# Kernel tuning notes

Measured on AMD Instinct MI355X. Metric: run time of the kernel, lower is better.

Reference implementation:

```python
import jax, jax.numpy as jnp
import numpy as np

NBITS = 8          # attn_nbits
GROUP = 32         # per-group size along head_dim for Q/K quantizers
H = 16             # num_heads
EPS = 1e-8


def _ste(x, q):
    # straight-through estimator: forward=q, backward=identity
    return x + jax.lax.stop_gradient(q - x)


def pg_dynamic_quant(x, group_size=GROUP, nbits=NBITS):
    """Per-group symmetric dynamic fake-quant along last dim (ActPGDynamicQuantizer)."""
    qmax = 2.0 ** (nbits - 1) - 1
    lead, D = x.shape[:-1], x.shape[-1]
    xg = x.reshape(*lead, D // group_size, group_size)
    s = jnp.maximum(jnp.max(jnp.abs(xg), axis=-1, keepdims=True) / qmax, EPS)
    q = jnp.clip(jnp.round(xg / s), -qmax - 1.0, qmax) * s
    return _ste(x, q.reshape(x.shape))


def dynamic_quant(x, axis=2, nbits=NBITS):
    """Symmetric dynamic fake-quant, scale shared along `axis` (ActDynamicQuantizer)."""
    qmax = 2.0 ** (nbits - 1) - 1
    s = jnp.maximum(jnp.max(jnp.abs(x), axis=axis, keepdims=True) / qmax, EPS)
    q = jnp.clip(jnp.round(x / s), -qmax - 1.0, qmax) * s
    return _ste(x, q)


def static_scale_quant(x, nbits=NBITS):
    """Unsigned static-scale fake-quant for softmax map in [0,1] (ActStaticScaleQuantizer)."""
    qmax = 2.0 ** nbits - 1
    q = jnp.clip(jnp.round(x * qmax), 0.0, qmax) / qmax
    return _ste(x, q)


def setup_inputs() -> dict:
    key = jax.random.key(0)
    ks = jax.random.split(key, 7)
    B, L, C = 4, 1024, 1024
    return {
        "x":         jax.random.normal(ks[0], (B, L, C), jnp.float32),
        "attn_bias": jax.random.normal(ks[1], (1, 1, L, L), jnp.float32) * 0.1,
        "w_qkv":     jax.random.normal(ks[2], (3 * C, C), jnp.float32) * 0.02,
        "q_bias":    jax.random.normal(ks[3], (C,), jnp.float32) * 0.02,
        "v_bias":    jax.random.normal(ks[4], (C,), jnp.float32) * 0.02,
        "w_proj":    jax.random.normal(ks[5], (C, C), jnp.float32) * 0.02,
        "b_proj":    jax.random.normal(ks[6], (C,), jnp.float32) * 0.02,
    }


def reference(x, attn_bias, w_qkv, q_bias, v_bias, w_proj, b_proj):
    B, L, C = x.shape
    D = C // H
    scale = D ** -0.5
    # qkv projection: bias-free linear + concat(q_bias, zeros_k, v_bias)
    bias = jnp.concatenate([q_bias, jnp.zeros_like(q_bias), v_bias])
    qkv = (x @ w_qkv.T + bias).reshape(B, L, 3, H, D)
    q, k, v = jnp.transpose(qkv, (2, 0, 3, 1, 4))  # each [B,H,L,D]
    # inline fake-quantization (MODE 0 inference path)
    qq = pg_dynamic_quant(q)
    kk = pg_dynamic_quant(k)
    vv = dynamic_quant(v, axis=2)
    attn = jnp.einsum('bhld,bhmd->bhlm', qq * scale, kk) + attn_bias  # [B,H,L,L]
    a = jax.nn.softmax(attn, axis=-1)
    a = static_scale_quant(a)
    out = jnp.einsum('bhlm,bhmd->bhld', a, vv)
    out = jnp.transpose(out, (0, 2, 1, 3)).reshape(B, L, C)
    return out @ w_proj.T + b_proj
```

## Files before the change

kernel.cpp:

```cpp
#include <hip/hip_runtime.h>


typedef unsigned short u16;
typedef unsigned int u32;
typedef __attribute__((ext_vector_type(8))) _Float16 half8;
typedef __attribute__((ext_vector_type(4))) float f32x4;

__device__ __forceinline__ u16 f2b(float f) {
    u32 i;
    __builtin_memcpy(&i, &f, 4);
    return (u16)((i + 0x7FFFu + ((i >> 16) & 1u)) >> 16);
}

__device__ __forceinline__ void split16(float v, u16& hi, u16& lo) {
    _Float16 h = (_Float16)v;
    _Float16 l = (_Float16)(v - (float)h);
    __builtin_memcpy(&hi, &h, 2);
    __builtin_memcpy(&lo, &l, 2);
}

__device__ __forceinline__ int dot4(int a, int b, int c) {
#if __has_builtin(__builtin_amdgcn_sdot4)
    return __builtin_amdgcn_sdot4(a, b, c, false);
#else
    int r = c;
    r += ((a << 24) >> 24) * ((b << 24) >> 24);
    r += ((a << 16) >> 24) * ((b << 16) >> 24);
    r += ((a << 8) >> 24) * ((b << 8) >> 24);
    r += (a >> 24) * (b >> 24);
    return r;
#endif
}

__global__ __launch_bounds__(256) void cvt_bf16w(u16* __restrict__ dst,
                                                 const float* __restrict__ src, int n) {
    int i = (blockIdx.x * 256 + threadIdx.x) * 4;
    if (i + 3 < n) {
        float4 v = *(const float4*)(src + i);
        ushort4 o;
        o.x = f2b(v.x); o.y = f2b(v.y); o.z = f2b(v.z); o.w = f2b(v.w);
        *(ushort4*)(dst + i) = o;
    }
}

__global__ __launch_bounds__(256) void gemm_qkv3(const float* __restrict__ A,
                                                 const float* __restrict__ Bm,
                                                 const float* __restrict__ qbias,
                                                 const float* __restrict__ vbias,
                                                 float* __restrict__ qws,
                                                 float* __restrict__ kws,
                                                 float* __restrict__ vws) {
    __shared__ u16 Ah[128 * 32], Al[128 * 32], Bh[128 * 32], Bl[128 * 32];
    const int t = threadIdx.x;
    const int lane = t & 63, w = t >> 6;
    const int wm = w >> 1, wn = w & 1;
    const int srow = t >> 2, scol = (t & 3) * 8;
    const int lm = lane & 15, lk = (lane >> 4) * 8;
    const int bm = blockIdx.y, bn = blockIdx.x;

    const float* ap = A + (size_t)(bm * 128 + srow) * 1024 + scol;
    const float* bp = Bm + (size_t)(bn * 128 + srow) * 1024 + scol;

    double dacc[4][4][4];
#pragma unroll
    for (int i = 0; i < 4; i++)
#pragma unroll
        for (int j = 0; j < 4; j++)
#pragma unroll
            for (int r = 0; r < 4; r++) dacc[i][j][r] = 0.0;

    for (int slab = 0; slab < 8; slab++) {
        f32x4 acc[4][4];
#pragma unroll
        for (int i = 0; i < 4; i++)
#pragma unroll
            for (int j = 0; j < 4; j++) acc[i][j] = (f32x4){0.f, 0.f, 0.f, 0.f};

        for (int kc = 0; kc < 4; kc++) {
            const int k0 = slab * 128 + kc * 32;
            float vreg[4][8];
#pragma unroll
            for (int e = 0; e < 4; e++) {
                const float* src = (e < 2) ? (ap + (e & 1) * (size_t)64 * 1024 + k0)
                                           : (bp + (e & 1) * (size_t)64 * 1024 + k0);
                float4 v0 = *(const float4*)(src);
                float4 v1 = *(const float4*)(src + 4);
                vreg[e][0] = v0.x; vreg[e][1] = v0.y; vreg[e][2] = v0.z; vreg[e][3] = v0.w;
                vreg[e][4] = v1.x; vreg[e][5] = v1.y; vreg[e][6] = v1.z; vreg[e][7] = v1.w;
            }
            __syncthreads();
#pragma unroll
            for (int e = 0; e < 4; e++) {
                union { u16 us[8]; uint4 v; } ph, pl;
#pragma unroll
                for (int j = 0; j < 8; j++) split16(vreg[e][j], ph.us[j], pl.us[j]);
                u16* dh = (e < 2) ? Ah : Bh;
                u16* dl = (e < 2) ? Al : Bl;
                int row = srow + (e & 1) * 64;
                *(uint4*)(dh + row * 32 + scol) = ph.v;
                *(uint4*)(dl + row * 32 + scol) = pl.v;
            }
            __syncthreads();

            half8 fah[4], fal[4], fbh[4], fbl[4];
#pragma unroll
            for (int i = 0; i < 4; i++) {
                int ra = (wm * 64 + i * 16 + lm) * 32 + lk;
                int rb = (wn * 64 + i * 16 + lm) * 32 + lk;
                fah[i] = *(const half8*)(Ah + ra);
                fal[i] = *(const half8*)(Al + ra);
                fbh[i] = *(const half8*)(Bh + rb);
                fbl[i] = *(const half8*)(Bl + rb);
            }
#pragma unroll
            for (int mi = 0; mi < 4; mi++)
#pragma unroll
                for (int ni = 0; ni < 4; ni++) {
                    acc[mi][ni] = __builtin_amdgcn_mfma_f32_16x16x32_f16(
                        fal[mi], fbh[ni], acc[mi][ni], 0, 0, 0);
                    acc[mi][ni] = __builtin_amdgcn_mfma_f32_16x16x32_f16(
                        fah[mi], fbl[ni], acc[mi][ni], 0, 0, 0);
                    acc[mi][ni] = __builtin_amdgcn_mfma_f32_16x16x32_f16(
                        fah[mi], fbh[ni], acc[mi][ni], 0, 0, 0);
                }
        }
#pragma unroll
        for (int i = 0; i < 4; i++)
#pragma unroll
            for (int j = 0; j < 4; j++)
#pragma unroll
                for (int r = 0; r < 4; r++) dacc[i][j][r] += (double)acc[i][j][r];
    }

    const int rbase = bm * 128 + wm * 64 + (lane >> 4) * 4;
    const int cbase = bn * 128 + wn * 64 + lm;
#pragma unroll
    for (int mi = 0; mi < 4; mi++)
#pragma unroll
        for (int ni = 0; ni < 4; ni++) {
            int col = cbase + ni * 16;
            int sel = col >> 10, cc = col & 1023;
            double bias = (sel == 0) ? (double)qbias[cc]
                        : ((sel == 2) ? (double)vbias[cc] : 0.0);
            float* dst = (sel == 0) ? qws : ((sel == 1) ? kws : vws);
#pragma unroll
            for (int r = 0; r < 4; r++) {
                int row = rbase + mi * 16 + r;
                dst[(size_t)row * 1024 + cc] = (float)(dacc[mi][ni][r] + bias);
            }
        }
}

__global__ __launch_bounds__(256) void quant_qk(const float* __restrict__ pre,
                                                signed char* __restrict__ qout,
                                                double* __restrict__ sout) {
    size_t g = (size_t)blockIdx.x * 256 + threadIdx.x;
    const float* p = pre + g * 32;
    float v[32];
    float amax = 0.f;
#pragma unroll
    for (int i = 0; i < 8; i++) {
        float4 q4 = ((const float4*)p)[i];
        v[i * 4 + 0] = q4.x; v[i * 4 + 1] = q4.y; v[i * 4 + 2] = q4.z; v[i * 4 + 3] = q4.w;
        amax = fmaxf(amax, fmaxf(fmaxf(fabsf(q4.x), fabsf(q4.y)),
                                 fmaxf(fabsf(q4.z), fabsf(q4.w))));
    }
    double s = fmax((double)amax / 127.0, 1e-8);
    sout[g] = s;
    int pk[8];
#pragma unroll
    for (int i = 0; i < 8; i++) {
        int b0 = (int)fmin(fmax(rint((double)v[i * 4 + 0] / s), -128.0), 127.0);
        int b1 = (int)fmin(fmax(rint((double)v[i * 4 + 1] / s), -128.0), 127.0);
        int b2 = (int)fmin(fmax(rint((double)v[i * 4 + 2] / s), -128.0), 127.0);
        int b3 = (int)fmin(fmax(rint((double)v[i * 4 + 3] / s), -128.0), 127.0);
        pk[i] = (b0 & 255) | ((b1 & 255) << 8) | ((b2 & 255) << 16) | ((b3 & 255) << 24);
    }
    int4* d = (int4*)(qout + g * 32);
    d[0] = make_int4(pk[0], pk[1], pk[2], pk[3]);
    d[1] = make_int4(pk[4], pk[5], pk[6], pk[7]);
}

__global__ __launch_bounds__(256) void quant_k(const float* __restrict__ pre,
                                               int* __restrict__ kT,
                                               double* __restrict__ ksT) {
    size_t g = (size_t)blockIdx.x * 256 + threadIdx.x;
    const float* p = pre + g * 32;
    float v[32];
    float amax = 0.f;
#pragma unroll
    for (int i = 0; i < 8; i++) {
        float4 q4 = ((const float4*)p)[i];
        v[i * 4 + 0] = q4.x; v[i * 4 + 1] = q4.y; v[i * 4 + 2] = q4.z; v[i * 4 + 3] = q4.w;
        amax = fmaxf(amax, fmaxf(fmaxf(fabsf(q4.x), fabsf(q4.y)),
                                 fmaxf(fabsf(q4.z), fabsf(q4.w))));
    }
    double s = fmax((double)amax / 127.0, 1e-8);
    int pk[8];
#pragma unroll
    for (int i = 0; i < 8; i++) {
        int b0 = (int)fmin(fmax(rint((double)v[i * 4 + 0] / s), -128.0), 127.0);
        int b1 = (int)fmin(fmax(rint((double)v[i * 4 + 1] / s), -128.0), 127.0);
        int b2 = (int)fmin(fmax(rint((double)v[i * 4 + 2] / s), -128.0), 127.0);
        int b3 = (int)fmin(fmax(rint((double)v[i * 4 + 3] / s), -128.0), 127.0);
        pk[i] = (b0 & 255) | ((b1 & 255) << 8) | ((b2 & 255) << 16) | ((b3 & 255) << 24);
    }
    const int m = (int)((g >> 5) & 1023);
    const int b = (int)(g >> 15);
    const int sub = (int)(g & 31);
    const int h = sub >> 1, pp = sub & 1;
    const int bh = b * 16 + h;
    int* dst = kT + ((size_t)bh * 16 + pp * 8) * 1024 + m;
#pragma unroll
    for (int i = 0; i < 8; i++) dst[i * 1024] = pk[i];
    ksT[((size_t)bh * 2 + pp) * 1024 + m] = s;
}

__global__ __launch_bounds__(256) void vmax_part(const float* __restrict__ vws,
                                                 float* __restrict__ pmax) {
    const int lc = blockIdx.x, b = blockIdx.y, t = threadIdx.x;
#pragma unroll
    for (int j = 0; j < 4; j++) {
        int cc = t + j * 256;
        float mx = 0.f;
        for (int l = 0; l < 64; l++)
            mx = fmaxf(mx, fabsf(vws[((size_t)(b * 1024 + lc * 64 + l)) * 1024 + cc]));
        pmax[(size_t)(b * 16 + lc) * 1024 + cc] = mx;
    }
}

__global__ __launch_bounds__(256) void vmax_final(const float* __restrict__ pmax,
                                                  double* __restrict__ vs) {
    int id = blockIdx.x * 256 + threadIdx.x;
    int b = id >> 10, cc = id & 1023;
    float mx = 0.f;
#pragma unroll
    for (int p = 0; p < 16; p++)
        mx = fmaxf(mx, pmax[(size_t)(b * 16 + p) * 1024 + cc]);
    vs[id] = fmax((double)mx / 127.0, 1e-8);
}

__global__ __launch_bounds__(256) void vquant(float* __restrict__ vws,
                                              const double* __restrict__ vs) {
    size_t e = ((size_t)blockIdx.x * 256 + threadIdx.x) * 4;
    int b = (int)(e >> 20), cc = (int)(e & 1023);
    float4 v = *(const float4*)(vws + e);
    double s0 = vs[b * 1024 + cc], s1 = vs[b * 1024 + cc + 1];
    double s2 = vs[b * 1024 + cc + 2], s3 = vs[b * 1024 + cc + 3];
    float4 o;
    o.x = (float)(fmin(fmax(rint((double)v.x / s0), -128.0), 127.0) * s0);
    o.y = (float)(fmin(fmax(rint((double)v.y / s1), -128.0), 127.0) * s1);
    o.z = (float)(fmin(fmax(rint((double)v.z / s2), -128.0), 127.0) * s2);
    o.w = (float)(fmin(fmax(rint((double)v.w / s3), -128.0), 127.0) * s3);
    *(float4*)(vws + e) = o;
}

__global__ __launch_bounds__(256) void attn(const signed char* __restrict__ qint,
                                            const int* __restrict__ kT,
                                            const double* __restrict__ qs,
                                            const double* __restrict__ ksT,
                                            const float* __restrict__ vfq,
                                            const float* __restrict__ abias,
                                            u16* __restrict__ ctx) {
    __shared__ int    kTs[16][256];
    __shared__ double ks0s[256], ks1s[256];
    __shared__ unsigned short sidx[4][512];
    __shared__ float  sval[4][512];
    const int t = threadIdx.x;
    const int wv = t >> 6, lane = t & 63;
    const int qt = blockIdx.x, h = blockIdx.y, b = blockIdx.z;
    const int row = qt * 4 + wv;
    const size_t qrow = (size_t)(b * 1024 + row);
    const int bh = b * 16 + h;

    const int* qv = (const int*)(qint + qrow * 1024 + h * 64);
    int qd[16];
#pragma unroll
    for (int j = 0; j < 4; j++) {
        int4 tmp = ((const int4*)qv)[j];
        qd[j * 4 + 0] = tmp.x; qd[j * 4 + 1] = tmp.y;
        qd[j * 4 + 2] = tmp.z; qd[j * 4 + 3] = tmp.w;
    }
    const double sq0 = qs[qrow * 32 + 2 * h], sq1 = qs[qrow * 32 + 2 * h + 1];
    const int* kTg = kT + (size_t)bh * 16384;
    const double* ks0g = ksT + (size_t)(bh * 2) * 1024;
    const double* ks1g = ksT + (size_t)(bh * 2 + 1) * 1024;
    const float* ab = abias + (size_t)row * 1024;

    double sd[16];
    for (int c = 0; c < 4; c++) {
        if (c) __syncthreads();
        {
            const int j = t >> 4, seg = t & 15;
            const int4* src = (const int4*)(kTg + j * 1024 + c * 256 + seg * 16);
            int4 a0 = src[0], a1 = src[1], a2 = src[2], a3 = src[3];
            int4* dst = (int4*)(&kTs[j][seg * 16]);
            dst[0] = a0; dst[1] = a1; dst[2] = a2; dst[3] = a3;
            ks0s[t] = ks0g[c * 256 + t];
            ks1s[t] = ks1g[c * 256 + t];
        }
        __syncthreads();
#pragma unroll
        for (int s = 0; s < 4; s++) {
            const int ml = s * 64 + lane;
            int I0 = 0, I1 = 0;
#pragma unroll
            for (int j = 0; j < 8; j++)  I0 = dot4(qd[j], kTs[j][ml], I0);
#pragma unroll
            for (int j = 8; j < 16; j++) I1 = dot4(qd[j], kTs[j][ml], I1);
            sd[c * 4 + s] = 0.125 * (sq0 * ks0s[ml] * (double)I0
                                   + sq1 * ks1s[ml] * (double)I1)
                          + (double)ab[c * 256 + ml];
        }
    }

    double mx = sd[0];
#pragma unroll
    for (int it = 1; it < 16; it++) mx = fmax(mx, sd[it]);
#pragma unroll
    for (int off = 1; off < 64; off <<= 1) mx = fmax(mx, __shfl_xor(mx, off));
    double sum = 0.0;
#pragma unroll
    for (int it = 0; it < 16; it++) {
        double e = exp(sd[it] - mx);
        sd[it] = e;
        sum += e;
    }
#pragma unroll
    for (int off = 1; off < 64; off <<= 1) sum += __shfl_xor(sum, off);

    int base = 0;
#pragma unroll
    for (int it = 0; it < 16; it++) {
        double a = sd[it] / sum;
        double n = fmin(fmax(rint(a * 255.0), 0.0), 255.0);
        float af = (float)(n / 255.0);
        unsigned long long mk = __ballot(af != 0.f);
        if (af != 0.f) {
            int pos = base + (int)__popcll(mk & ((1ull << lane) - 1ull));
            sidx[wv][pos] = (unsigned short)(it * 64 + lane);
            sval[wv][pos] = af;
        }
        base += (int)__popcll(mk);
    }
    __syncthreads();

    float acc = 0.f;
    const float* vcol = vfq + ((size_t)b * 1024) * 1024 + h * 64 + lane;
    for (int j = 0; j < base; ++j) {
        int m = sidx[wv][j];
        float a = sval[wv][j];
        acc = fmaf(a, vcol[(size_t)m * 1024], acc);
    }
    ctx[qrow * 1024 + h * 64 + lane] = f2b(acc);
}

__global__ __launch_bounds__(256) void gemm_proj(const u16* __restrict__ ctx,
                                                 const u16* __restrict__ wproj,
                                                 const float* __restrict__ bproj,
                                                 float* __restrict__ out) {
    typedef __attribute__((ext_vector_type(8))) short short8;
    __shared__ u16 As[128 * 32], Bs[128 * 32];
    f32x4 acc[4][4];
#pragma unroll
    for (int i = 0; i < 4; i++)
#pragma unroll
        for (int j = 0; j < 4; j++) acc[i][j] = (f32x4){0.f, 0.f, 0.f, 0.f};

    const int t = threadIdx.x;
    const int lane = t & 63, w = t >> 6;
    const int wm = w >> 1, wn = w & 1;
    const int srow = t >> 2, scol = (t & 3) * 8;
    const int lm = lane & 15, lk = (lane >> 4) * 8;
    const int bm = blockIdx.y, bn = blockIdx.x;
    const u16* ap = ctx + (size_t)(bm * 128 + srow) * 1024 + scol;
    const u16* bp = wproj + (size_t)(bn * 128 + srow) * 1024 + scol;

    for (int k0 = 0; k0 < 1024; k0 += 32) {
        uint4 a0 = *(const uint4*)(ap + k0);
        uint4 a1 = *(const uint4*)(ap + (size_t)64 * 1024 + k0);
        uint4 b0 = *(const uint4*)(bp + k0);
        uint4 b1 = *(const uint4*)(bp + (size_t)64 * 1024 + k0);
        __syncthreads();
        *(uint4*)(As + srow * 32 + scol) = a0;
        *(uint4*)(As + (srow + 64) * 32 + scol) = a1;
        *(uint4*)(Bs + srow * 32 + scol) = b0;
        *(uint4*)(Bs + (srow + 64) * 32 + scol) = b1;
        __syncthreads();
        short8 af[4], bfr[4];
#pragma unroll
        for (int i = 0; i < 4; i++) {
            af[i]  = *(const short8*)(As + (wm * 64 + i * 16 + lm) * 32 + lk);
            bfr[i] = *(const short8*)(Bs + (wn * 64 + i * 16 + lm) * 32 + lk);
        }
#pragma unroll
        for (int mi = 0; mi < 4; mi++)
#pragma unroll
            for (int ni = 0; ni < 4; ni++)
                acc[mi][ni] = __builtin_amdgcn_mfma_f32_16x16x32_bf16(
                    af[mi], bfr[ni], acc[mi][ni], 0, 0, 0);
    }

    const int rbase = bm * 128 + wm * 64 + (lane >> 4) * 4;
    const int cbase = bn * 128 + wn * 64 + lm;
#pragma unroll
    for (int mi = 0; mi < 4; mi++)
#pragma unroll
        for (int ni = 0; ni < 4; ni++) {
            int col = cbase + ni * 16;
            float bias = bproj[col];
#pragma unroll
            for (int r = 0; r < 4; r++) {
                int row = rbase + mi * 16 + r;
                out[(size_t)row * 1024 + col] = acc[mi][ni][r] + bias;
            }
        }
}

extern "C" void kernel_launch(void* const* d_in, const int* in_sizes, int n_in,
                              void* d_out, int out_size, void* d_ws, size_t ws_size,
                              hipStream_t stream) {
    const float* x     = (const float*)d_in[0];
    const float* abias = (const float*)d_in[1];
    const float* wqkv  = (const float*)d_in[2];
    const float* qbias = (const float*)d_in[3];
    const float* vbias = (const float*)d_in[4];
    const float* wproj = (const float*)d_in[5];
    const float* bproj = (const float*)d_in[6];
    float* out = (float*)d_out;

    char* ws = (char*)d_ws;
    float*       qpre    = (float*)(ws + 0);
    float*       kpre    = (float*)(ws + 16777216);
    float*       vfq     = (float*)(ws + 33554432);
    u16*         wprojbf = (u16*)  (ws + 50331648);
    signed char* qint    = (signed char*)(ws + 52428800);
    int*         kT      = (int*)  (ws + 56623104);
    double*      qs      = (double*)(ws + 60817408);
    double*      ksT     = (double*)(ws + 61865984);
    double*      vs      = (double*)(ws + 62914560);
    float*       pmax    = (float*)(ws + 62947328);
    u16*         ctx     = (u16*)(ws + 0);

    cvt_bf16w<<<1024, 256, 0, stream>>>(wprojbf, wproj, 1048576);
    gemm_qkv3<<<dim3(24, 32), 256, 0, stream>>>(x, wqkv, qbias, vbias,
                                                qpre, kpre, vfq);
    quant_qk<<<512, 256, 0, stream>>>(qpre, qint, qs);
    quant_k<<<512, 256, 0, stream>>>(kpre, kT, ksT);
    vmax_part<<<dim3(16, 4), 256, 0, stream>>>(vfq, pmax);
    vmax_final<<<16, 256, 0, stream>>>(pmax, vs);
    vquant<<<4096, 256, 0, stream>>>(vfq, vs);
    attn<<<dim3(256, 16, 4), 256, 0, stream>>>(qint, kT, qs, ksT, vfq, abias, ctx);
    gemm_proj<<<dim3(8, 32), 256, 0, stream>>>(ctx, wprojbf, bproj, out);
}
```

Measured before the change: 586.5 us.

## Interleave quantized K as int4 per key and drop LDS staging in attention

Quantized K is rewritten into an interleaved layout so each key's 16 packed int8 words sit in four int4 groups. The attention kernel then reads K and the K scales straight from global memory per lane, removing the LDS tile staging and the block-wide barriers in the score loop. The sparse softmax index and value lists are packed into one u32 per entry, cutting LDS use, which may raise occupancy. The cost is that every wave now loads K from global or cache on its own instead of sharing one tile across the block.

Result: slower. 650.6 us (+10.9%).

```diff
diff --git a/kernel.cpp b/kernel.cpp
--- a/kernel.cpp
+++ b/kernel.cpp
@@ -210,9 +210,9 @@
     const int sub = (int)(g & 31);
     const int h = sub >> 1, pp = sub & 1;
     const int bh = b * 16 + h;
-    int* dst = kT + ((size_t)bh * 16 + pp * 8) * 1024 + m;
-#pragma unroll
-    for (int i = 0; i < 8; i++) dst[i * 1024] = pk[i];
+    int* dst = kT + (((size_t)bh * 4 + pp * 2) * 1024 + m) * 4;
+#pragma unroll
+    for (int i = 0; i < 8; i++) dst[(i >> 2) * 4096 + (i & 3)] = pk[i];
     ksT[((size_t)bh * 2 + pp) * 1024 + m] = s;
 }
 
@@ -256,16 +256,13 @@
 }
 
 __global__ __launch_bounds__(256) void attn(const signed char* __restrict__ qint,
-                                            const int* __restrict__ kT,
+                                            const int* __restrict__ kT4,
                                             const double* __restrict__ qs,
                                             const double* __restrict__ ksT,
                                             const float* __restrict__ vfq,
                                             const float* __restrict__ abias,
                                             u16* __restrict__ ctx) {
-    __shared__ int    kTs[16][256];
-    __shared__ double ks0s[256], ks1s[256];
-    __shared__ unsigned short sidx[4][512];
-    __shared__ float  sval[4][512];
+    __shared__ u32 packed[4][512];
     const int t = threadIdx.x;
     const int wv = t >> 6, lane = t & 63;
     const int qt = blockIdx.x, h = blockIdx.y, b = blockIdx.z;
@@ -282,36 +279,31 @@
         qd[j * 4 + 2] = tmp.z; qd[j * 4 + 3] = tmp.w;
     }
     const double sq0 = qs[qrow * 32 + 2 * h], sq1 = qs[qrow * 32 + 2 * h + 1];
-    const int* kTg = kT + (size_t)bh * 16384;
+    const int4* kB = (const int4*)kT4 + (size_t)bh * 4096;
     const double* ks0g = ksT + (size_t)(bh * 2) * 1024;
     const double* ks1g = ksT + (size_t)(bh * 2 + 1) * 1024;
     const float* ab = abias + (size_t)row * 1024;
 
     double sd[16];
-    for (int c = 0; c < 4; c++) {
-        if (c) __syncthreads();
-        {
-            const int j = t >> 4, seg = t & 15;
-            const int4* src = (const int4*)(kTg + j * 1024 + c * 256 + seg * 16);
-            int4 a0 = src[0], a1 = src[1], a2 = src[2], a3 = src[3];
-            int4* dst = (int4*)(&kTs[j][seg * 16]);
-            dst[0] = a0; dst[1] = a1; dst[2] = a2; dst[3] = a3;
-            ks0s[t] = ks0g[c * 256 + t];
-            ks1s[t] = ks1g[c * 256 + t];
-        }
-        __syncthreads();
-#pragma unroll
-        for (int s = 0; s < 4; s++) {
-            const int ml = s * 64 + lane;
-            int I0 = 0, I1 = 0;
-#pragma unroll
-            for (int j = 0; j < 8; j++)  I0 = dot4(qd[j], kTs[j][ml], I0);
-#pragma unroll
-            for (int j = 8; j < 16; j++) I1 = dot4(qd[j], kTs[j][ml], I1);
-            sd[c * 4 + s] = 0.125 * (sq0 * ks0s[ml] * (double)I0
-                                   + sq1 * ks1s[ml] * (double)I1)
-                          + (double)ab[c * 256 + ml];
-        }
+#pragma unroll
+    for (int it = 0; it < 16; it++) {
+        const int m = it * 64 + lane;
+        int4 k0 = kB[m];
+        int4 k1 = kB[1024 + m];
+        int4 k2 = kB[2048 + m];
+        int4 k3 = kB[3072 + m];
+        int I0 = 0, I1 = 0;
+        I0 = dot4(qd[0], k0.x, I0);  I0 = dot4(qd[1], k0.y, I0);
+        I0 = dot4(qd[2], k0.z, I0);  I0 = dot4(qd[3], k0.w, I0);
+        I0 = dot4(qd[4], k1.x, I0);  I0 = dot4(qd[5], k1.y, I0);
+        I0 = dot4(qd[6], k1.z, I0);  I0 = dot4(qd[7], k1.w, I0);
+        I1 = dot4(qd[8], k2.x, I1);  I1 = dot4(qd[9], k2.y, I1);
+        I1 = dot4(qd[10], k2.z, I1); I1 = dot4(qd[11], k2.w, I1);
+        I1 = dot4(qd[12], k3.x, I1); I1 = dot4(qd[13], k3.y, I1);
+        I1 = dot4(qd[14], k3.z, I1); I1 = dot4(qd[15], k3.w, I1);
+        sd[it] = 0.125 * (sq0 * ks0g[m] * (double)I0
+                        + sq1 * ks1g[m] * (double)I1)
+               + (double)ab[m];
     }
 
     double mx = sd[0];
@@ -333,13 +325,12 @@
 #pragma unroll
     for (int it = 0; it < 16; it++) {
         double a = sd[it] / sum;
-        double n = fmin(fmax(rint(a * 255.0), 0.0), 255.0);
-        float af = (float)(n / 255.0);
-        unsigned long long mk = __ballot(af != 0.f);
-        if (af != 0.f) {
+        double nd = fmin(fmax(rint(a * 255.0), 0.0), 255.0);
+        int ni = (int)nd;
+        unsigned long long mk = __ballot(ni != 0);
+        if (ni != 0) {
             int pos = base + (int)__popcll(mk & ((1ull << lane) - 1ull));
-            sidx[wv][pos] = (unsigned short)(it * 64 + lane);
-            sval[wv][pos] = af;
+            packed[wv][pos] = ((u32)ni << 16) | (u32)(it * 64 + lane);
         }
         base += (int)__popcll(mk);
     }
@@ -348,9 +339,9 @@
     float acc = 0.f;
     const float* vcol = vfq + ((size_t)b * 1024) * 1024 + h * 64 + lane;
     for (int j = 0; j < base; ++j) {
-        int m = sidx[wv][j];
-        float a = sval[wv][j];
-        acc = fmaf(a, vcol[(size_t)m * 1024], acc);
+        u32 p = packed[wv][j];
+        float a = (float)(p >> 16) / 255.0f;
+        acc = fmaf(a, vcol[(size_t)(p & 1023u) * 1024], acc);
     }
     ctx[qrow * 1024 + h * 64 + lane] = f2b(acc);
 }
@@ -435,7 +426,7 @@
     float*       vfq     = (float*)(ws + 33554432);
     u16*         wprojbf = (u16*)  (ws + 50331648);
     signed char* qint    = (signed char*)(ws + 52428800);
-    int*         kT      = (int*)  (ws + 56623104);
+    int*         kT4     = (int*)  (ws + 56623104);
     double*      qs      = (double*)(ws + 60817408);
     double*      ksT     = (double*)(ws + 61865984);
     double*      vs      = (double*)(ws + 62914560);
@@ -446,10 +437,10 @@
     gemm_qkv3<<<dim3(24, 32), 256, 0, stream>>>(x, wqkv, qbias, vbias,
                                                 qpre, kpre, vfq);
     quant_qk<<<512, 256, 0, stream>>>(qpre, qint, qs);
-    quant_k<<<512, 256, 0, stream>>>(kpre, kT, ksT);
+    quant_k<<<512, 256, 0, stream>>>(kpre, kT4, ksT);
     vmax_part<<<dim3(16, 4), 256, 0, stream>>>(vfq, pmax);
     vmax_final<<<16, 256, 0, stream>>>(pmax, vs);
     vquant<<<4096, 256, 0, stream>>>(vfq, vs);
-    attn<<<dim3(256, 16, 4), 256, 0, stream>>>(qint, kT, qs, ksT, vfq, abias, ctx);
+    attn<<<dim3(256, 16, 4), 256, 0, stream>>>(qint, kT4, qs, ksT, vfq, abias, ctx);
     gemm_proj<<<dim3(8, 32), 256, 0, stream>>>(ctx, wprojbf, bproj, out);
 }
```
